# Kernel optimization log

Hardware: AMD Instinct MI355X
Metric: run time of the kernel (lower is better)

## Reference

```python
import jax, jax.numpy as jnp
import numpy as np

EPS = 1e-5

def _bn(x, g, b, m, v):
    # inference-mode BatchNorm2d over NCHW
    inv = g / jnp.sqrt(v + EPS)
    return x * inv[None, :, None, None] + (b - m * inv)[None, :, None, None]

def _adder2d(x, w, stride, pad):
    # AdderNet 'convolution': out = -sum_{c,kh,kw} |patch - w|
    B, C, H, W = x.shape
    O, _, k, _ = w.shape
    xp = jnp.pad(x, ((0, 0), (0, 0), (pad, pad), (pad, pad)))
    Ho = (H + 2 * pad - k) // stride + 1
    Wo = (W + 2 * pad - k) // stride + 1
    # unfold: [B, C, k*k, Ho, Wo] with (C, kh, kw) ordering matching w.reshape
    cols = jnp.stack([xp[:, :, i:i + stride * Ho:stride, j:j + stride * Wo:stride]
                      for i in range(k) for j in range(k)], axis=2)
    cols = cols.reshape(B, C * k * k, Ho * Wo)            # [B, CKK, L]
    wf = w.reshape(O, C * k * k)                          # [O, CKK]
    out = -jnp.sum(jnp.abs(cols[:, None, :, :] - wf[None, :, :, None]), axis=2)  # [B,O,L]
    return out.reshape(B, O, Ho, Wo)

def setup_inputs() -> dict:
    key = jax.random.key(0)
    ks = jax.random.split(key, 16)
    C = 64
    return {
        "x": jax.random.normal(ks[0], (4, C, 32, 32), jnp.float32),
        "bn1_g": jax.random.uniform(ks[1], (C,), jnp.float32),
        "bn1_b": jax.random.normal(ks[2], (C,), jnp.float32),
        "bn1_m": jax.random.normal(ks[3], (C,), jnp.float32),
        "bn1_v": jax.random.uniform(ks[4], (C,), jnp.float32),
        "w1": jax.random.normal(ks[5], (C, C, 3, 3), jnp.float32),
        "bn2_g": jax.random.uniform(ks[6], (C,), jnp.float32),
        "bn2_b": jax.random.normal(ks[7], (C,), jnp.float32),
        "bn2_m": jax.random.normal(ks[8], (C,), jnp.float32),
        "bn2_v": jax.random.uniform(ks[9], (C,), jnp.float32),
        "w2": jax.random.normal(ks[10], (C, C, 3, 3), jnp.float32),
        "fc1_w": jax.random.normal(ks[11], (C // 16, C), jnp.float32) * 0.1,
        "fc1_b": jax.random.normal(ks[12], (C // 16,), jnp.float32) * 0.1,
        "fc2_w": jax.random.normal(ks[13], (C, C // 16), jnp.float32) * 0.1,
        "fc2_b": jax.random.normal(ks[14], (C,), jnp.float32) * 0.1,
    }

def reference(x, bn1_g, bn1_b, bn1_m, bn1_v, w1,
              bn2_g, bn2_b, bn2_m, bn2_v, w2,
              fc1_w, fc1_b, fc2_w, fc2_b):
    out = jax.nn.relu(_bn(x, bn1_g, bn1_b, bn1_m, bn1_v))
    shortcut = x  # stride==1 and in_planes==planes -> identity shortcut
    out = _adder2d(out, w1, 1, 1)
    out = _adder2d(jax.nn.relu(_bn(out, bn2_g, bn2_b, bn2_m, bn2_v)), w2, 1, 1)
    # SE gate: global avg pool -> fc1 -> relu -> fc2 -> sigmoid
    s = out.mean(axis=(2, 3))                              # [B, planes]
    h = jax.nn.relu(s @ fc1_w.T + fc1_b)
    g = jax.nn.sigmoid(h @ fc2_w.T + fc2_b)
    return out * g[:, :, None, None] + shortcut
```

## Files before the change

### kernel.cpp

```cpp
#include <hip/hip_runtime.h>
#include <math.h>

#define NELEM   262144
#define NPAIRW  18432
#define PIMG    1296
#define PPADN   165888
#define NPAIR   147968
#define EPS_BN  1e-5f
#define QSC     128.0f
#define QBIAS_F 16384.5f
#define QZ_W    0x40004000u
#define QINV    (1.0f / 128.0f)

__device__ __forceinline__ unsigned sad16(unsigned a, unsigned b, unsigned acc) {
    asm("v_sad_u16 %0, %1, %2, %0" : "+v"(acc) : "v"(a), "v"(b));
    return acc;
}
__device__ __forceinline__ unsigned qu(float v) {
    return (unsigned)(int)fmaf(v, QSC, QBIAS_F);
}

__global__ __launch_bounds__(256) void prep_kernel(
    const float* __restrict__ x,
    const float* __restrict__ g1, const float* __restrict__ b1,
    const float* __restrict__ m1, const float* __restrict__ v1,
    const float* __restrict__ w1,
    const float* __restrict__ g2, const float* __restrict__ b2,
    const float* __restrict__ m2, const float* __restrict__ v2,
    const float* __restrict__ w2,
    unsigned* __restrict__ qxp, unsigned* __restrict__ qout1p,
    unsigned* __restrict__ qw1p, unsigned* __restrict__ qw2p,
    float* __restrict__ bn2c, float* __restrict__ sbuf)
{
    int i = blockIdx.x * 256 + threadIdx.x;
    if (i < NPAIR) {
        int bp  = i / 1156;
        int rc  = i - bp * 1156;
        int r   = rc / 34;
        int col = rc - r * 34;
        bool interior = (r > 0 && r < 33 && col > 0 && col < 33);
        unsigned q = QZ_W;
        if (interior) {
            int b  = bp >> 5;
            int c0 = (bp & 31) * 2;
            float inv0 = g1[c0] * rsqrtf(v1[c0] + EPS_BN);
            float bet0 = b1[c0] - m1[c0] * inv0;
            float inv1 = g1[c0 + 1] * rsqrtf(v1[c0 + 1] + EPS_BN);
            float bet1 = b1[c0 + 1] - m1[c0 + 1] * inv1;
            int off = (b * 64 + c0) * 1024 + (r - 1) * 32 + (col - 1);
            float a0 = fmaxf(fmaf(x[off],        inv0, bet0), 0.f);
            float a1 = fmaxf(fmaf(x[off + 1024], inv1, bet1), 0.f);
            q = qu(a0) | (qu(a1) << 16);
        }
        int pidx = bp * PIMG + r * 36 + col;
        qxp[pidx] = q;
        if (!interior) qout1p[pidx] = QZ_W;
        return;
    }
    int k = i - NPAIR;
    if (k < NPAIRW) {
        int o   = k / 288;
        int rem = k - o * 288;
        int pr  = rem / 9;
        int kk  = rem - pr * 9;
        int woff = (o * 64 + pr * 2) * 9 + kk;
        qw1p[k] = qu(w1[woff]) | (qu(w1[woff + 9]) << 16);
        return;
    }
    int l = k - NPAIRW;
    if (l < NPAIRW) {
        int o   = l / 288;
        int rem = l - o * 288;
        int pr  = rem / 9;
        int kk  = rem - pr * 9;
        int woff = (o * 64 + pr * 2) * 9 + kk;
        qw2p[l] = qu(w2[woff]) | (qu(w2[woff + 9]) << 16);
        return;
    }
    int m = l - NPAIRW;
    if (m < 64) {
        float inv = g2[m] * rsqrtf(v2[m] + EPS_BN);
        bn2c[m]      = -inv * QINV;
        bn2c[m + 64] = b2[m] - m2[m] * inv;
        return;
    }
    int s = m - 64;
    if (s >= 0 && s < 256) sbuf[s] = 0.f;
}

template<int MODE>
__global__ __launch_bounds__(256, 4) void adder_kernel(
    const unsigned* __restrict__ qsrc, const unsigned* __restrict__ qwp,
    const float* __restrict__ bn2c,
    unsigned* __restrict__ qout, float* __restrict__ fout,
    float* __restrict__ sbuf)
{
    __shared__ unsigned wlds[2][32][12];
    __shared__ unsigned red[8][32][9];

    const int blk = blockIdx.x;
    const int sp  = blk & 7;
    const int og  = (blk >> 3) & 31;
    const int b   = blk >> 8;
    const int t   = threadIdx.x;
    const int pos = t & 31;
    const int cq  = t >> 5;
    const int y_i = pos >> 3;
    const int x0  = (pos & 7) * 4;

    for (int i = t; i < 576; i += 256) {
        int o_i = i / 288;
        int rem = i - o_i * 288;
        int pr  = rem / 9;
        int kk  = rem - pr * 9;
        wlds[o_i][pr][kk] = qwp[((og * 2 + o_i) * 32 + pr) * 9 + kk];
    }
    __syncthreads();

    unsigned acc[2][4];
#pragma unroll
    for (int oo = 0; oo < 2; ++oo)
#pragma unroll
        for (int xi = 0; xi < 4; ++xi) acc[oo][xi] = 0u;

#pragma unroll
    for (int j = 0; j < 4; ++j) {
        const int pr = cq * 4 + j;
        const unsigned* pc = qsrc + (size_t)(b * 32 + pr) * PIMG
                                  + (sp * 4 + y_i) * 36 + x0;
        unsigned p[3][6];
#pragma unroll
        for (int r = 0; r < 3; ++r) {
            uint4 a0 = *reinterpret_cast<const uint4*>(pc + r * 36);
            uint2 a1 = *reinterpret_cast<const uint2*>(pc + r * 36 + 4);
            p[r][0] = a0.x; p[r][1] = a0.y; p[r][2] = a0.z; p[r][3] = a0.w;
            p[r][4] = a1.x; p[r][5] = a1.y;
        }
#pragma unroll
        for (int oo = 0; oo < 2; ++oo) {
            uint4 wa = *reinterpret_cast<const uint4*>(&wlds[oo][pr][0]);
            uint4 wb = *reinterpret_cast<const uint4*>(&wlds[oo][pr][4]);
            unsigned w8 = wlds[oo][pr][8];
            unsigned wv[9] = {wa.x, wa.y, wa.z, wa.w,
                              wb.x, wb.y, wb.z, wb.w, w8};
#pragma unroll
            for (int kh = 0; kh < 3; ++kh)
#pragma unroll
                for (int kw = 0; kw < 3; ++kw) {
                    unsigned ww = wv[kh * 3 + kw];
#pragma unroll
                    for (int xi = 0; xi < 4; ++xi)
                        acc[oo][xi] = sad16(p[kh][xi + kw], ww, acc[oo][xi]);
                }
        }
    }

    {
        unsigned* dst = &red[cq][pos][0];
#pragma unroll
        for (int z = 0; z < 8; ++z) dst[z] = acc[z >> 2][z & 3];
    }
    __syncthreads();

    const int oo2 = t >> 7;
    const int yy2 = (t >> 5) & 3;
    const int xx2 = t & 31;
    const int pp  = yy2 * 8 + (xx2 >> 2);
    const int z   = oo2 * 4 + (xx2 & 3);
    unsigned total = 0;
#pragma unroll
    for (int q = 0; q < 8; ++q) total += red[q][pp][z];

    const int o  = og * 2 + oo2;
    const int gy = sp * 4 + yy2;

    if (MODE == 0) {
        float a2 = fmaxf(fmaf((float)total, bn2c[o], bn2c[o + 64]), 0.f);
        unsigned short qv = (unsigned short)(int)fmaf(a2, QSC, QBIAS_F);
        size_t widx = (size_t)(b * 32 + (o >> 1)) * PIMG + (gy + 1) * 36 + (xx2 + 1);
        reinterpret_cast<unsigned short*>(qout)[widx * 2 + (o & 1)] = qv;
    } else {
        float v = -(float)total * QINV;
        fout[((b * 64 + o) * 32 + gy) * 32 + xx2] = v;
        float sum = v;
#pragma unroll
        for (int off = 32; off > 0; off >>= 1)
            sum += __shfl_down(sum, off, 64);
        if ((t & 63) == 0) atomicAdd(&sbuf[b * 64 + o], sum);
    }
}

__global__ __launch_bounds__(256) void gate_kernel(
    const float* __restrict__ out2, const float* __restrict__ x,
    const float* __restrict__ sbuf,
    const float* __restrict__ fc1w, const float* __restrict__ fc1b,
    const float* __restrict__ fc2w, const float* __restrict__ fc2b,
    float* __restrict__ out)
{
    const int bo = blockIdx.x;
    const int b  = bo >> 6;
    const int o  = bo & 63;
    const int t  = threadIdx.x;

    __shared__ float ss[64];
    if (t < 64) ss[t] = sbuf[b * 64 + t] * (1.f / 1024.f);
    __syncthreads();

    float h[4];
#pragma unroll
    for (int j = 0; j < 4; ++j) {
        float a = fc1b[j];
#pragma unroll
        for (int c = 0; c < 64; ++c) a += ss[c] * fc1w[j * 64 + c];
        h[j] = fmaxf(a, 0.f);
    }
    float zz = fc2b[o];
#pragma unroll
    for (int j = 0; j < 4; ++j) zz += h[j] * fc2w[o * 4 + j];
    float g = 1.f / (1.f + __expf(-zz));

    const int base = bo * 1024 + t * 4;
    float4 v  = *reinterpret_cast<const float4*>(out2 + base);
    float4 xv = *reinterpret_cast<const float4*>(x + base);
    float4 r;
    r.x = v.x * g + xv.x;
    r.y = v.y * g + xv.y;
    r.z = v.z * g + xv.z;
    r.w = v.w * g + xv.w;
    *reinterpret_cast<float4*>(out + base) = r;
}

extern "C" void kernel_launch(void* const* d_in, const int* in_sizes, int n_in,
                              void* d_out, int out_size, void* d_ws, size_t ws_size,
                              hipStream_t stream)
{
    const float* x    = (const float*)d_in[0];
    const float* bn1g = (const float*)d_in[1];
    const float* bn1b = (const float*)d_in[2];
    const float* bn1m = (const float*)d_in[3];
    const float* bn1v = (const float*)d_in[4];
    const float* w1   = (const float*)d_in[5];
    const float* bn2g = (const float*)d_in[6];
    const float* bn2b = (const float*)d_in[7];
    const float* bn2m = (const float*)d_in[8];
    const float* bn2v = (const float*)d_in[9];
    const float* w2   = (const float*)d_in[10];
    const float* fc1w = (const float*)d_in[11];
    const float* fc1b = (const float*)d_in[12];
    const float* fc2w = (const float*)d_in[13];
    const float* fc2b = (const float*)d_in[14];

    unsigned* ws     = (unsigned*)d_ws;
    unsigned* qxp    = ws;
    unsigned* qout1p = ws + PPADN;
    float*    out2   = (float*)(ws + 2 * PPADN);
    unsigned* qw1p   = ws + 2 * PPADN + NELEM;
    unsigned* qw2p   = ws + 2 * PPADN + NELEM + NPAIRW;
    float*    bn2c   = (float*)(ws + 2 * PPADN + NELEM + 2 * NPAIRW);
    float*    sbuf   = (float*)(ws + 2 * PPADN + NELEM + 2 * NPAIRW + 128);

    prep_kernel<<<724, 256, 0, stream>>>(x, bn1g, bn1b, bn1m, bn1v, w1,
                                         bn2g, bn2b, bn2m, bn2v, w2,
                                         qxp, qout1p, qw1p, qw2p, bn2c, sbuf);
    adder_kernel<0><<<1024, 256, 0, stream>>>(qxp,    qw1p, bn2c, qout1p, nullptr, nullptr);
    adder_kernel<1><<<1024, 256, 0, stream>>>(qout1p, qw2p, nullptr, nullptr, out2, sbuf);
    gate_kernel<<<256, 256, 0, stream>>>(out2, x, sbuf, fc1w, fc1b, fc2w, fc2b,
                                         (float*)d_out);
}
```

Before: 109.4 us.

## Fuse input prep and weight quantization into adder kernels, dropping prep launch

Removes the separate prep kernel. The first adder kernel now applies BN1, ReLU and quantization to its own input rows directly into shared memory, and quantizes its weights on load. It also computes the BN2 constants inline, writes the output halo and zeroes the SE sum buffer. The second adder kernel quantizes w2 on load. This saves one launch and the round-trip of the quantized input and weights through global memory, in exchange for redundant per-block recomputation of BN and quantization work and more shared memory in the first kernel.

```diff
diff --git a/kernel.cpp b/kernel.cpp
--- a/kernel.cpp
+++ b/kernel.cpp
@@ -2,10 +2,9 @@
 #include <math.h>
 
 #define NELEM   262144
-#define NPAIRW  18432
 #define PIMG    1296
 #define PPADN   165888
-#define NPAIR   147968
+#define NHALO   16896
 #define EPS_BN  1e-5f
 #define QSC     128.0f
 #define QBIAS_F 16384.5f
@@ -20,80 +19,159 @@
     return (unsigned)(int)fmaf(v, QSC, QBIAS_F);
 }
 
-__global__ __launch_bounds__(256) void prep_kernel(
+__global__ __launch_bounds__(256, 4) void adder1_kernel(
     const float* __restrict__ x,
     const float* __restrict__ g1, const float* __restrict__ b1,
     const float* __restrict__ m1, const float* __restrict__ v1,
     const float* __restrict__ w1,
     const float* __restrict__ g2, const float* __restrict__ b2,
     const float* __restrict__ m2, const float* __restrict__ v2,
-    const float* __restrict__ w2,
-    unsigned* __restrict__ qxp, unsigned* __restrict__ qout1p,
-    unsigned* __restrict__ qw1p, unsigned* __restrict__ qw2p,
-    float* __restrict__ bn2c, float* __restrict__ sbuf)
+    unsigned* __restrict__ qout, float* __restrict__ sbuf)
 {
-    int i = blockIdx.x * 256 + threadIdx.x;
-    if (i < NPAIR) {
-        int bp  = i / 1156;
-        int rc  = i - bp * 1156;
-        int r   = rc / 34;
-        int col = rc - r * 34;
-        bool interior = (r > 0 && r < 33 && col > 0 && col < 33);
-        unsigned q = QZ_W;
-        if (interior) {
-            int b  = bp >> 5;
-            int c0 = (bp & 31) * 2;
-            float inv0 = g1[c0] * rsqrtf(v1[c0] + EPS_BN);
-            float bet0 = b1[c0] - m1[c0] * inv0;
-            float inv1 = g1[c0 + 1] * rsqrtf(v1[c0 + 1] + EPS_BN);
-            float bet1 = b1[c0 + 1] - m1[c0 + 1] * inv1;
-            int off = (b * 64 + c0) * 1024 + (r - 1) * 32 + (col - 1);
-            float a0 = fmaxf(fmaf(x[off],        inv0, bet0), 0.f);
-            float a1 = fmaxf(fmaf(x[off + 1024], inv1, bet1), 0.f);
-            q = qu(a0) | (qu(a1) << 16);
-        }
-        int pidx = bp * PIMG + r * 36 + col;
-        qxp[pidx] = q;
-        if (!interior) qout1p[pidx] = QZ_W;
-        return;
-    }
-    int k = i - NPAIR;
-    if (k < NPAIRW) {
-        int o   = k / 288;
-        int rem = k - o * 288;
+    __shared__ unsigned smem[7680];
+    unsigned (*xs)[6][36]    = reinterpret_cast<unsigned(*)[6][36]>(smem);
+    unsigned (*red)[32][9]   = reinterpret_cast<unsigned(*)[32][9]>(smem);
+    unsigned (*wlds)[32][12] = reinterpret_cast<unsigned(*)[32][12]>(smem + 6912);
+
+    const int blk = blockIdx.x;
+    const int sp  = blk & 7;
+    const int og  = (blk >> 3) & 31;
+    const int b   = blk >> 8;
+    const int t   = threadIdx.x;
+
+    const int gid = blk * 256 + t;
+    if (gid < 256) sbuf[gid] = 0.f;
+    if (gid < NHALO) {
+        int img = gid / 132;
+        int j   = gid - img * 132;
+        int r, c;
+        if (j < 34)       { r = 0;          c = j;       }
+        else if (j < 68)  { r = 33;         c = j - 34;  }
+        else if (j < 100) { r = j - 68 + 1; c = 0;       }
+        else              { r = j - 100 + 1; c = 33;     }
+        qout[img * PIMG + r * 36 + c] = QZ_W;
+    }
+
+    for (int i = t; i < 576; i += 256) {
+        int o_i = i / 288;
+        int rem = i - o_i * 288;
         int pr  = rem / 9;
         int kk  = rem - pr * 9;
-        int woff = (o * 64 + pr * 2) * 9 + kk;
-        qw1p[k] = qu(w1[woff]) | (qu(w1[woff + 9]) << 16);
-        return;
-    }
-    int l = k - NPAIRW;
-    if (l < NPAIRW) {
-        int o   = l / 288;
-        int rem = l - o * 288;
-        int pr  = rem / 9;
-        int kk  = rem - pr * 9;
-        int woff = (o * 64 + pr * 2) * 9 + kk;
-        qw2p[l] = qu(w2[woff]) | (qu(w2[woff + 9]) << 16);
-        return;
-    }
-    int m = l - NPAIRW;
-    if (m < 64) {
-        float inv = g2[m] * rsqrtf(v2[m] + EPS_BN);
-        bn2c[m]      = -inv * QINV;
-        bn2c[m + 64] = b2[m] - m2[m] * inv;
-        return;
-    }
-    int s = m - 64;
-    if (s >= 0 && s < 256) sbuf[s] = 0.f;
-}
-
-template<int MODE>
-__global__ __launch_bounds__(256, 4) void adder_kernel(
-    const unsigned* __restrict__ qsrc, const unsigned* __restrict__ qwp,
-    const float* __restrict__ bn2c,
-    unsigned* __restrict__ qout, float* __restrict__ fout,
-    float* __restrict__ sbuf)
+        int woff = ((og * 2 + o_i) * 64 + pr * 2) * 9 + kk;
+        wlds[o_i][pr][kk] = qu(w1[woff]) | (qu(w1[woff + 9]) << 16);
+    }
+
+    for (int u = t; u < 192; u += 256) {
+        const int pair = u / 6;
+        const int lr   = u - pair * 6;
+        const int xrow = sp * 4 + lr - 1;
+        unsigned* dst  = &xs[pair][lr][0];
+        if (xrow < 0 || xrow > 31) {
+#pragma unroll
+            for (int k = 0; k < 9; ++k)
+                reinterpret_cast<uint4*>(dst)[k] = make_uint4(QZ_W, QZ_W, QZ_W, QZ_W);
+        } else {
+            const int c0 = pair * 2;
+            const float inv0 = g1[c0]     * rsqrtf(v1[c0]     + EPS_BN);
+            const float bet0 = b1[c0]     - m1[c0]     * inv0;
+            const float inv1 = g1[c0 + 1] * rsqrtf(v1[c0 + 1] + EPS_BN);
+            const float bet1 = b1[c0 + 1] - m1[c0 + 1] * inv1;
+            const float* x0p = x + ((b * 64 + c0) * 32 + xrow) * 32;
+            const float* x1p = x0p + 1024;
+#pragma unroll
+            for (int k = 0; k < 9; ++k) {
+                unsigned q[4];
+#pragma unroll
+                for (int e = 0; e < 4; ++e) {
+                    int c = k * 4 + e;
+                    unsigned qv = QZ_W;
+                    if (c >= 1 && c <= 32) {
+                        float a0 = fmaxf(fmaf(x0p[c - 1], inv0, bet0), 0.f);
+                        float a1 = fmaxf(fmaf(x1p[c - 1], inv1, bet1), 0.f);
+                        qv = qu(a0) | (qu(a1) << 16);
+                    }
+                    q[e] = qv;
+                }
+                reinterpret_cast<uint4*>(dst)[k] = make_uint4(q[0], q[1], q[2], q[3]);
+            }
+        }
+    }
+    __syncthreads();
+
+    const int pos = t & 31;
+    const int cq  = t >> 5;
+    const int y_i = pos >> 3;
+    const int x0  = (pos & 7) * 4;
+
+    unsigned acc[2][4];
+#pragma unroll
+    for (int oo = 0; oo < 2; ++oo)
+#pragma unroll
+        for (int xi = 0; xi < 4; ++xi) acc[oo][xi] = 0u;
+
+#pragma unroll
+    for (int j = 0; j < 4; ++j) {
+        const int pr = cq * 4 + j;
+        unsigned p[3][6];
+#pragma unroll
+        for (int r = 0; r < 3; ++r) {
+            const unsigned* src = &xs[pr][y_i + r][x0];
+            uint4 a0 = *reinterpret_cast<const uint4*>(src);
+            uint2 a1 = *reinterpret_cast<const uint2*>(src + 4);
+            p[r][0] = a0.x; p[r][1] = a0.y; p[r][2] = a0.z; p[r][3] = a0.w;
+            p[r][4] = a1.x; p[r][5] = a1.y;
+        }
+#pragma unroll
+        for (int oo = 0; oo < 2; ++oo) {
+            uint4 wa = *reinterpret_cast<const uint4*>(&wlds[oo][pr][0]);
+            uint4 wb = *reinterpret_cast<const uint4*>(&wlds[oo][pr][4]);
+            unsigned w8 = wlds[oo][pr][8];
+            unsigned wv[9] = {wa.x, wa.y, wa.z, wa.w,
+                              wb.x, wb.y, wb.z, wb.w, w8};
+#pragma unroll
+            for (int kh = 0; kh < 3; ++kh)
+#pragma unroll
+                for (int kw = 0; kw < 3; ++kw) {
+                    unsigned ww = wv[kh * 3 + kw];
+#pragma unroll
+                    for (int xi = 0; xi < 4; ++xi)
+                        acc[oo][xi] = sad16(p[kh][xi + kw], ww, acc[oo][xi]);
+                }
+        }
+    }
+    __syncthreads();
+
+    {
+        unsigned* dst = &red[cq][pos][0];
+#pragma unroll
+        for (int z = 0; z < 8; ++z) dst[z] = acc[z >> 2][z & 3];
+    }
+    __syncthreads();
+
+    const int oo2 = t >> 7;
+    const int yy2 = (t >> 5) & 3;
+    const int xx2 = t & 31;
+    const int pp  = yy2 * 8 + (xx2 >> 2);
+    const int z   = oo2 * 4 + (xx2 & 3);
+    unsigned total = 0;
+#pragma unroll
+    for (int q = 0; q < 8; ++q) total += red[q][pp][z];
+
+    const int o  = og * 2 + oo2;
+    const int gy = sp * 4 + yy2;
+
+    float inv = g2[o] * rsqrtf(v2[o] + EPS_BN);
+    float cc0 = -inv * QINV;
+    float cc1 = b2[o] - m2[o] * inv;
+    float a2  = fmaxf(fmaf((float)total, cc0, cc1), 0.f);
+    unsigned short qv = (unsigned short)(int)fmaf(a2, QSC, QBIAS_F);
+    size_t widx = (size_t)(b * 32 + (o >> 1)) * PIMG + (gy + 1) * 36 + (xx2 + 1);
+    reinterpret_cast<unsigned short*>(qout)[widx * 2 + (o & 1)] = qv;
+}
+
+__global__ __launch_bounds__(256, 4) void adder2_kernel(
+    const unsigned* __restrict__ qsrc, const float* __restrict__ w2,
+    float* __restrict__ fout, float* __restrict__ sbuf)
 {
     __shared__ unsigned wlds[2][32][12];
     __shared__ unsigned red[8][32][9];
@@ -113,7 +191,8 @@
         int rem = i - o_i * 288;
         int pr  = rem / 9;
         int kk  = rem - pr * 9;
-        wlds[o_i][pr][kk] = qwp[((og * 2 + o_i) * 32 + pr) * 9 + kk];
+        int woff = ((og * 2 + o_i) * 64 + pr * 2) * 9 + kk;
+        wlds[o_i][pr][kk] = qu(w2[woff]) | (qu(w2[woff + 9]) << 16);
     }
     __syncthreads();
 
@@ -174,20 +253,13 @@
     const int o  = og * 2 + oo2;
     const int gy = sp * 4 + yy2;
 
-    if (MODE == 0) {
-        float a2 = fmaxf(fmaf((float)total, bn2c[o], bn2c[o + 64]), 0.f);
-        unsigned short qv = (unsigned short)(int)fmaf(a2, QSC, QBIAS_F);
-        size_t widx = (size_t)(b * 32 + (o >> 1)) * PIMG + (gy + 1) * 36 + (xx2 + 1);
-        reinterpret_cast<unsigned short*>(qout)[widx * 2 + (o & 1)] = qv;
-    } else {
-        float v = -(float)total * QINV;
-        fout[((b * 64 + o) * 32 + gy) * 32 + xx2] = v;
-        float sum = v;
-#pragma unroll
-        for (int off = 32; off > 0; off >>= 1)
-            sum += __shfl_down(sum, off, 64);
-        if ((t & 63) == 0) atomicAdd(&sbuf[b * 64 + o], sum);
-    }
+    float v = -(float)total * QINV;
+    fout[((b * 64 + o) * 32 + gy) * 32 + xx2] = v;
+    float sum = v;
+#pragma unroll
+    for (int off = 32; off > 0; off >>= 1)
+        sum += __shfl_down(sum, off, 64);
+    if ((t & 63) == 0) atomicAdd(&sbuf[b * 64 + o], sum);
 }
 
 __global__ __launch_bounds__(256) void gate_kernel(
@@ -251,19 +323,14 @@
     const float* fc2b = (const float*)d_in[14];
 
     unsigned* ws     = (unsigned*)d_ws;
-    unsigned* qxp    = ws;
-    unsigned* qout1p = ws + PPADN;
-    float*    out2   = (float*)(ws + 2 * PPADN);
-    unsigned* qw1p   = ws + 2 * PPADN + NELEM;
-    unsigned* qw2p   = ws + 2 * PPADN + NELEM + NPAIRW;
-    float*    bn2c   = (float*)(ws + 2 * PPADN + NELEM + 2 * NPAIRW);
-    float*    sbuf   = (float*)(ws + 2 * PPADN + NELEM + 2 * NPAIRW + 128);
-
-    prep_kernel<<<724, 256, 0, stream>>>(x, bn1g, bn1b, bn1m, bn1v, w1,
-                                         bn2g, bn2b, bn2m, bn2v, w2,
-                                         qxp, qout1p, qw1p, qw2p, bn2c, sbuf);
-    adder_kernel<0><<<1024, 256, 0, stream>>>(qxp,    qw1p, bn2c, qout1p, nullptr, nullptr);
-    adder_kernel<1><<<1024, 256, 0, stream>>>(qout1p, qw2p, nullptr, nullptr, out2, sbuf);
+    unsigned* qout1p = ws;
+    float*    out2   = (float*)(ws + PPADN);
+    float*    sbuf   = (float*)(ws + PPADN + NELEM);
+
+    adder1_kernel<<<1024, 256, 0, stream>>>(x, bn1g, bn1b, bn1m, bn1v, w1,
+                                            bn2g, bn2b, bn2m, bn2v,
+                                            qout1p, sbuf);
+    adder2_kernel<<<1024, 256, 0, stream>>>(qout1p, w2, out2, sbuf);
     gate_kernel<<<256, 256, 0, stream>>>(out2, x, sbuf, fc1w, fc1b, fc2w, fc2b,
                                          (float*)d_out);
 }
```

After: 114.7 us. 1.05x slower.

## Fuse all four kernels into one persistent kernel with grid barriers

Applied to the files above, without the earlier changes.

Merges the prep, both adder passes and the SE gate into a single 1024-block kernel separated by atomic-counter grid barriers, with a memset to reset the counters and the pooled sums. It also folds the BN2 constant computation into the first adder epilogue. The aim is to remove the launch gaps between kernels. The barriers assume all 1024 blocks are co-resident (256 CUs × 4 blocks), otherwise the kernel deadlocks, and the spin-wait plus memset add their own overhead.

```diff
diff --git a/kernel.cpp b/kernel.cpp
--- a/kernel.cpp
+++ b/kernel.cpp
@@ -1,6 +1,7 @@
 #include <hip/hip_runtime.h>
 #include <math.h>
 
+#define GRIDN   1024
 #define NELEM   262144
 #define NPAIRW  18432
 #define PIMG    1296
@@ -20,7 +21,121 @@
     return (unsigned)(int)fmaf(v, QSC, QBIAS_F);
 }
 
-__global__ __launch_bounds__(256) void prep_kernel(
+__device__ __forceinline__ void gridbar(unsigned* cnt, int t) {
+    __syncthreads();
+    if (t == 0) {
+        __threadfence();
+        __hip_atomic_fetch_add(cnt, 1u, __ATOMIC_ACQ_REL, __HIP_MEMORY_SCOPE_AGENT);
+        while (__hip_atomic_load(cnt, __ATOMIC_RELAXED, __HIP_MEMORY_SCOPE_AGENT) < GRIDN)
+            __builtin_amdgcn_s_sleep(2);
+        __threadfence();
+    }
+    __syncthreads();
+}
+
+template<int MODE>
+__device__ __forceinline__ void adder_phase(
+    unsigned (*wlds)[32][12], unsigned (*red)[32][9],
+    const unsigned* __restrict__ qsrc, const unsigned* __restrict__ qwp,
+    const float* __restrict__ g2, const float* __restrict__ b2,
+    const float* __restrict__ m2, const float* __restrict__ v2,
+    unsigned* __restrict__ qout, float* __restrict__ fout,
+    float* __restrict__ sbuf, int blk, int t)
+{
+    const int sp  = blk & 7;
+    const int og  = (blk >> 3) & 31;
+    const int b   = blk >> 8;
+    const int pos = t & 31;
+    const int cq  = t >> 5;
+    const int y_i = pos >> 3;
+    const int x0  = (pos & 7) * 4;
+
+    for (int i = t; i < 576; i += 256) {
+        int o_i = i / 288;
+        int rem = i - o_i * 288;
+        int pr  = rem / 9;
+        int kk  = rem - pr * 9;
+        wlds[o_i][pr][kk] = qwp[((og * 2 + o_i) * 32 + pr) * 9 + kk];
+    }
+    __syncthreads();
+
+    unsigned acc[2][4];
+#pragma unroll
+    for (int oo = 0; oo < 2; ++oo)
+#pragma unroll
+        for (int xi = 0; xi < 4; ++xi) acc[oo][xi] = 0u;
+
+#pragma unroll
+    for (int j = 0; j < 4; ++j) {
+        const int pr = cq * 4 + j;
+        const unsigned* pc = qsrc + (size_t)(b * 32 + pr) * PIMG
+                                  + (sp * 4 + y_i) * 36 + x0;
+        unsigned p[3][6];
+#pragma unroll
+        for (int r = 0; r < 3; ++r) {
+            uint4 a0 = *reinterpret_cast<const uint4*>(pc + r * 36);
+            uint2 a1 = *reinterpret_cast<const uint2*>(pc + r * 36 + 4);
+            p[r][0] = a0.x; p[r][1] = a0.y; p[r][2] = a0.z; p[r][3] = a0.w;
+            p[r][4] = a1.x; p[r][5] = a1.y;
+        }
+#pragma unroll
+        for (int oo = 0; oo < 2; ++oo) {
+            uint4 wa = *reinterpret_cast<const uint4*>(&wlds[oo][pr][0]);
+            uint4 wb = *reinterpret_cast<const uint4*>(&wlds[oo][pr][4]);
+            unsigned w8 = wlds[oo][pr][8];
+            unsigned wv[9] = {wa.x, wa.y, wa.z, wa.w,
+                              wb.x, wb.y, wb.z, wb.w, w8};
+#pragma unroll
+            for (int kh = 0; kh < 3; ++kh)
+#pragma unroll
+                for (int kw = 0; kw < 3; ++kw) {
+                    unsigned ww = wv[kh * 3 + kw];
+#pragma unroll
+                    for (int xi = 0; xi < 4; ++xi)
+                        acc[oo][xi] = sad16(p[kh][xi + kw], ww, acc[oo][xi]);
+                }
+        }
+    }
+
+    {
+        unsigned* dst = &red[cq][pos][0];
+#pragma unroll
+        for (int z = 0; z < 8; ++z) dst[z] = acc[z >> 2][z & 3];
+    }
+    __syncthreads();
+
+    const int oo2 = t >> 7;
+    const int yy2 = (t >> 5) & 3;
+    const int xx2 = t & 31;
+    const int pp  = yy2 * 8 + (xx2 >> 2);
+    const int z   = oo2 * 4 + (xx2 & 3);
+    unsigned total = 0;
+#pragma unroll
+    for (int q = 0; q < 8; ++q) total += red[q][pp][z];
+
+    const int o  = og * 2 + oo2;
+    const int gy = sp * 4 + yy2;
+
+    if (MODE == 0) {
+        float inv = g2[o] * rsqrtf(v2[o] + EPS_BN);
+        float cc0 = -inv * QINV;
+        float cc1 = b2[o] - m2[o] * inv;
+        float a2  = fmaxf(fmaf((float)total, cc0, cc1), 0.f);
+        unsigned short qv = (unsigned short)(int)fmaf(a2, QSC, QBIAS_F);
+        size_t widx = (size_t)(b * 32 + (o >> 1)) * PIMG + (gy + 1) * 36 + (xx2 + 1);
+        reinterpret_cast<unsigned short*>(qout)[widx * 2 + (o & 1)] = qv;
+    } else {
+        float v = -(float)total * QINV;
+        fout[((b * 64 + o) * 32 + gy) * 32 + xx2] = v;
+        float sum = v;
+#pragma unroll
+        for (int off = 32; off > 0; off >>= 1)
+            sum += __shfl_down(sum, off, 64);
+        if ((t & 63) == 0) atomicAdd(&sbuf[b * 64 + o], sum);
+    }
+}
+
+__global__ __launch_bounds__(256, 4) void fused_kernel(
     const float* __restrict__ x,
     const float* __restrict__ g1, const float* __restrict__ b1,
     const float* __restrict__ m1, const float* __restrict__ v1,
@@ -28,206 +143,108 @@
     const float* __restrict__ g2, const float* __restrict__ b2,
     const float* __restrict__ m2, const float* __restrict__ v2,
     const float* __restrict__ w2,
+    const float* __restrict__ fc1w, const float* __restrict__ fc1b,
+    const float* __restrict__ fc2w, const float* __restrict__ fc2b,
+    float* __restrict__ sbuf, unsigned* __restrict__ cnt,
     unsigned* __restrict__ qxp, unsigned* __restrict__ qout1p,
     unsigned* __restrict__ qw1p, unsigned* __restrict__ qw2p,
-    float* __restrict__ bn2c, float* __restrict__ sbuf)
+    float* __restrict__ out2, float* __restrict__ out)
 {
-    int i = blockIdx.x * 256 + threadIdx.x;
-    if (i < NPAIR) {
-        int bp  = i / 1156;
-        int rc  = i - bp * 1156;
-        int r   = rc / 34;
-        int col = rc - r * 34;
-        bool interior = (r > 0 && r < 33 && col > 0 && col < 33);
-        unsigned q = QZ_W;
-        if (interior) {
-            int b  = bp >> 5;
-            int c0 = (bp & 31) * 2;
-            float inv0 = g1[c0] * rsqrtf(v1[c0] + EPS_BN);
-            float bet0 = b1[c0] - m1[c0] * inv0;
-            float inv1 = g1[c0 + 1] * rsqrtf(v1[c0 + 1] + EPS_BN);
-            float bet1 = b1[c0 + 1] - m1[c0 + 1] * inv1;
-            int off = (b * 64 + c0) * 1024 + (r - 1) * 32 + (col - 1);
-            float a0 = fmaxf(fmaf(x[off],        inv0, bet0), 0.f);
-            float a1 = fmaxf(fmaf(x[off + 1024], inv1, bet1), 0.f);
-            q = qu(a0) | (qu(a1) << 16);
-        }
-        int pidx = bp * PIMG + r * 36 + col;
-        qxp[pidx] = q;
-        if (!interior) qout1p[pidx] = QZ_W;
-        return;
-    }
-    int k = i - NPAIR;
-    if (k < NPAIRW) {
-        int o   = k / 288;
-        int rem = k - o * 288;
-        int pr  = rem / 9;
-        int kk  = rem - pr * 9;
-        int woff = (o * 64 + pr * 2) * 9 + kk;
-        qw1p[k] = qu(w1[woff]) | (qu(w1[woff + 9]) << 16);
-        return;
-    }
-    int l = k - NPAIRW;
-    if (l < NPAIRW) {
-        int o   = l / 288;
-        int rem = l - o * 288;
-        int pr  = rem / 9;
-        int kk  = rem - pr * 9;
-        int woff = (o * 64 + pr * 2) * 9 + kk;
-        qw2p[l] = qu(w2[woff]) | (qu(w2[woff + 9]) << 16);
-        return;
-    }
-    int m = l - NPAIRW;
-    if (m < 64) {
-        float inv = g2[m] * rsqrtf(v2[m] + EPS_BN);
-        bn2c[m]      = -inv * QINV;
-        bn2c[m + 64] = b2[m] - m2[m] * inv;
-        return;
-    }
-    int s = m - 64;
-    if (s >= 0 && s < 256) sbuf[s] = 0.f;
-}
-
-template<int MODE>
-__global__ __launch_bounds__(256, 4) void adder_kernel(
-    const unsigned* __restrict__ qsrc, const unsigned* __restrict__ qwp,
-    const float* __restrict__ bn2c,
-    unsigned* __restrict__ qout, float* __restrict__ fout,
-    float* __restrict__ sbuf)
-{
-    __shared__ unsigned wlds[2][32][12];
-    __shared__ unsigned red[8][32][9];
+    __shared__ unsigned smem[3072];
+    unsigned (*wlds)[32][12] = reinterpret_cast<unsigned(*)[32][12]>(smem);
+    unsigned (*red)[32][9]   = reinterpret_cast<unsigned(*)[32][9]>(smem + 768);
 
     const int blk = blockIdx.x;
-    const int sp  = blk & 7;
-    const int og  = (blk >> 3) & 31;
-    const int b   = blk >> 8;
     const int t   = threadIdx.x;
-    const int pos = t & 31;
-    const int cq  = t >> 5;
-    const int y_i = pos >> 3;
-    const int x0  = (pos & 7) * 4;
-
-    for (int i = t; i < 576; i += 256) {
-        int o_i = i / 288;
-        int rem = i - o_i * 288;
-        int pr  = rem / 9;
-        int kk  = rem - pr * 9;
-        wlds[o_i][pr][kk] = qwp[((og * 2 + o_i) * 32 + pr) * 9 + kk];
-    }
-    __syncthreads();
-
-    unsigned acc[2][4];
-#pragma unroll
-    for (int oo = 0; oo < 2; ++oo)
-#pragma unroll
-        for (int xi = 0; xi < 4; ++xi) acc[oo][xi] = 0u;
-
-#pragma unroll
-    for (int j = 0; j < 4; ++j) {
-        const int pr = cq * 4 + j;
-        const unsigned* pc = qsrc + (size_t)(b * 32 + pr) * PIMG
-                                  + (sp * 4 + y_i) * 36 + x0;
-        unsigned p[3][6];
-#pragma unroll
-        for (int r = 0; r < 3; ++r) {
-            uint4 a0 = *reinterpret_cast<const uint4*>(pc + r * 36);
-            uint2 a1 = *reinterpret_cast<const uint2*>(pc + r * 36 + 4);
-            p[r][0] = a0.x; p[r][1] = a0.y; p[r][2] = a0.z; p[r][3] = a0.w;
-            p[r][4] = a1.x; p[r][5] = a1.y;
-        }
-#pragma unroll
-        for (int oo = 0; oo < 2; ++oo) {
-            uint4 wa = *reinterpret_cast<const uint4*>(&wlds[oo][pr][0]);
-            uint4 wb = *reinterpret_cast<const uint4*>(&wlds[oo][pr][4]);
-            unsigned w8 = wlds[oo][pr][8];
-            unsigned wv[9] = {wa.x, wa.y, wa.z, wa.w,
-                              wb.x, wb.y, wb.z, wb.w, w8};
-#pragma unroll
-            for (int kh = 0; kh < 3; ++kh)
-#pragma unroll
-                for (int kw = 0; kw < 3; ++kw) {
-                    unsigned ww = wv[kh * 3 + kw];
-#pragma unroll
-                    for (int xi = 0; xi < 4; ++xi)
-                        acc[oo][xi] = sad16(p[kh][xi + kw], ww, acc[oo][xi]);
+
+    {
+        int i = blk * 256 + t;
+        if (i < NPAIR) {
+            int bp  = i / 1156;
+            int rc  = i - bp * 1156;
+            int r   = rc / 34;
+            int col = rc - r * 34;
+            bool interior = (r > 0 && r < 33 && col > 0 && col < 33);
+            unsigned q = QZ_W;
+            if (interior) {
+                int b  = bp >> 5;
+                int c0 = (bp & 31) * 2;
+                float inv0 = g1[c0] * rsqrtf(v1[c0] + EPS_BN);
+                float bet0 = b1[c0] - m1[c0] * inv0;
+                float inv1 = g1[c0 + 1] * rsqrtf(v1[c0 + 1] + EPS_BN);
+                float bet1 = b1[c0 + 1] - m1[c0 + 1] * inv1;
+                int off = (b * 64 + c0) * 1024 + (r - 1) * 32 + (col - 1);
+                float a0 = fmaxf(fmaf(x[off],        inv0, bet0), 0.f);
+                float a1 = fmaxf(fmaf(x[off + 1024], inv1, bet1), 0.f);
+                q = qu(a0) | (qu(a1) << 16);
+            }
+            int pidx = bp * PIMG + r * 36 + col;
+            qxp[pidx] = q;
+            if (!interior) qout1p[pidx] = QZ_W;
+        } else {
+            int k = i - NPAIR;
+            if (k < NPAIRW) {
+                int o   = k / 288;
+                int rem = k - o * 288;
+                int pr  = rem / 9;
+                int kk  = rem - pr * 9;
+                int woff = (o * 64 + pr * 2) * 9 + kk;
+                qw1p[k] = qu(w1[woff]) | (qu(w1[woff + 9]) << 16);
+            } else {
+                int l = k - NPAIRW;
+                if (l < NPAIRW) {
+                    int o   = l / 288;
+                    int rem = l - o * 288;
+                    int pr  = rem / 9;
+                    int kk  = rem - pr * 9;
+                    int woff = (o * 64 + pr * 2) * 9 + kk;
+                    qw2p[l] = qu(w2[woff]) | (qu(w2[woff + 9]) << 16);
                 }
-        }
-    }
-
-    {
-        unsigned* dst = &red[cq][pos][0];
-#pragma unroll
-        for (int z = 0; z < 8; ++z) dst[z] = acc[z >> 2][z & 3];
-    }
-    __syncthreads();
-
-    const int oo2 = t >> 7;
-    const int yy2 = (t >> 5) & 3;
-    const int xx2 = t & 31;
-    const int pp  = yy2 * 8 + (xx2 >> 2);
-    const int z   = oo2 * 4 + (xx2 & 3);
-    unsigned total = 0;
-#pragma unroll
-    for (int q = 0; q < 8; ++q) total += red[q][pp][z];
-
-    const int o  = og * 2 + oo2;
-    const int gy = sp * 4 + yy2;
-
-    if (MODE == 0) {
-        float a2 = fmaxf(fmaf((float)total, bn2c[o], bn2c[o + 64]), 0.f);
-        unsigned short qv = (unsigned short)(int)fmaf(a2, QSC, QBIAS_F);
-        size_t widx = (size_t)(b * 32 + (o >> 1)) * PIMG + (gy + 1) * 36 + (xx2 + 1);
-        reinterpret_cast<unsigned short*>(qout)[widx * 2 + (o & 1)] = qv;
-    } else {
-        float v = -(float)total * QINV;
-        fout[((b * 64 + o) * 32 + gy) * 32 + xx2] = v;
-        float sum = v;
-#pragma unroll
-        for (int off = 32; off > 0; off >>= 1)
-            sum += __shfl_down(sum, off, 64);
-        if ((t & 63) == 0) atomicAdd(&sbuf[b * 64 + o], sum);
-    }
-}
-
-__global__ __launch_bounds__(256) void gate_kernel(
-    const float* __restrict__ out2, const float* __restrict__ x,
-    const float* __restrict__ sbuf,
-    const float* __restrict__ fc1w, const float* __restrict__ fc1b,
-    const float* __restrict__ fc2w, const float* __restrict__ fc2b,
-    float* __restrict__ out)
-{
-    const int bo = blockIdx.x;
-    const int b  = bo >> 6;
-    const int o  = bo & 63;
-    const int t  = threadIdx.x;
-
-    __shared__ float ss[64];
-    if (t < 64) ss[t] = sbuf[b * 64 + t] * (1.f / 1024.f);
-    __syncthreads();
-
-    float h[4];
-#pragma unroll
-    for (int j = 0; j < 4; ++j) {
-        float a = fc1b[j];
-#pragma unroll
-        for (int c = 0; c < 64; ++c) a += ss[c] * fc1w[j * 64 + c];
-        h[j] = fmaxf(a, 0.f);
-    }
-    float zz = fc2b[o];
-#pragma unroll
-    for (int j = 0; j < 4; ++j) zz += h[j] * fc2w[o * 4 + j];
-    float g = 1.f / (1.f + __expf(-zz));
-
-    const int base = bo * 1024 + t * 4;
-    float4 v  = *reinterpret_cast<const float4*>(out2 + base);
-    float4 xv = *reinterpret_cast<const float4*>(x + base);
-    float4 r;
-    r.x = v.x * g + xv.x;
-    r.y = v.y * g + xv.y;
-    r.z = v.z * g + xv.z;
-    r.w = v.w * g + xv.w;
-    *reinterpret_cast<float4*>(out + base) = r;
+            }
+        }
+    }
+    gridbar(cnt + 0, t);
+
+    adder_phase<0>(wlds, red, qxp, qw1p, g2, b2, m2, v2,
+                   qout1p, nullptr, nullptr, blk, t);
+    gridbar(cnt + 16, t);
+
+    adder_phase<1>(wlds, red, qout1p, qw2p, nullptr, nullptr, nullptr, nullptr,
+                   nullptr, out2, sbuf, blk, t);
+    gridbar(cnt + 32, t);
+
+    if (blk < 256) {
+        const int bo = blk;
+        const int b  = bo >> 6;
+        const int o  = bo & 63;
+
+        float* ss = reinterpret_cast<float*>(smem);
+        if (t < 64) ss[t] = sbuf[b * 64 + t] * (1.f / 1024.f);
+        __syncthreads();
+
+        float h[4];
+#pragma unroll
+        for (int j = 0; j < 4; ++j) {
+            float a = fc1b[j];
+#pragma unroll
+            for (int c = 0; c < 64; ++c) a += ss[c] * fc1w[j * 64 + c];
+            h[j] = fmaxf(a, 0.f);
+        }
+        float zz = fc2b[o];
+#pragma unroll
+        for (int j = 0; j < 4; ++j) zz += h[j] * fc2w[o * 4 + j];
+        float g = 1.f / (1.f + __expf(-zz));
+
+        const int base = bo * 1024 + t * 4;
+        float4 v  = *reinterpret_cast<const float4*>(out2 + base);
+        float4 xv = *reinterpret_cast<const float4*>(x + base);
+        float4 r;
+        r.x = v.x * g + xv.x;
+        r.y = v.y * g + xv.y;
+        r.z = v.z * g + xv.z;
+        r.w = v.w * g + xv.w;
+        *reinterpret_cast<float4*>(out + base) = r;
+    }
 }
 
 extern "C" void kernel_launch(void* const* d_in, const int* in_sizes, int n_in,
@@ -251,19 +268,19 @@
     const float* fc2b = (const float*)d_in[14];
 
     unsigned* ws     = (unsigned*)d_ws;
-    unsigned* qxp    = ws;
-    unsigned* qout1p = ws + PPADN;
-    float*    out2   = (float*)(ws + 2 * PPADN);
-    unsigned* qw1p   = ws + 2 * PPADN + NELEM;
-    unsigned* qw2p   = ws + 2 * PPADN + NELEM + NPAIRW;
-    float*    bn2c   = (float*)(ws + 2 * PPADN + NELEM + 2 * NPAIRW);
-    float*    sbuf   = (float*)(ws + 2 * PPADN + NELEM + 2 * NPAIRW + 128);
-
-    prep_kernel<<<724, 256, 0, stream>>>(x, bn1g, bn1b, bn1m, bn1v, w1,
-                                         bn2g, bn2b, bn2m, bn2v, w2,
-                                         qxp, qout1p, qw1p, qw2p, bn2c, sbuf);
-    adder_kernel<0><<<1024, 256, 0, stream>>>(qxp,    qw1p, bn2c, qout1p, nullptr, nullptr);
-    adder_kernel<1><<<1024, 256, 0, stream>>>(qout1p, qw2p, nullptr, nullptr, out2, sbuf);
-    gate_kernel<<<256, 256, 0, stream>>>(out2, x, sbuf, fc1w, fc1b, fc2w, fc2b,
-                                         (float*)d_out);
-}
+    float*    sbuf   = (float*)ws;
+    unsigned* cnt    = ws + 256;
+    unsigned* qxp    = ws + 512;
+    unsigned* qout1p = ws + 512 + PPADN;
+    unsigned* qw1p   = ws + 512 + 2 * PPADN;
+    unsigned* qw2p   = ws + 512 + 2 * PPADN + NPAIRW;
+    float*    out2   = (float*)(ws + 512 + 2 * PPADN + 2 * NPAIRW);
+
+    hipMemsetAsync(d_ws, 0, 512 * sizeof(unsigned), stream);
+
+    fused_kernel<<<GRIDN, 256, 0, stream>>>(
+        x, bn1g, bn1b, bn1m, bn1v, w1,
+        bn2g, bn2b, bn2m, bn2v, w2,
+        fc1w, fc1b, fc2w, fc2b,
+        sbuf, cnt, qxp, qout1p, qw1p, qw2p, out2, (float*)d_out);
+}
```

Measured after the change: 371.7 us. +239.6%, slower.
